# Kernel optimization log

Hardware: AMD Instinct MI355X
Metric: run time of the kernel (lower is better)

Reference implementation:

```python
import jax, jax.numpy as jnp
import numpy as np

EMBED = 1024

def setup_inputs() -> dict:
    key = jax.random.key(0)
    ks = jax.random.split(key, 10)
    s = 1.0 / np.sqrt(EMBED)
    inp = {
        "target": jax.random.normal(ks[0], (8, 2048, EMBED), dtype=jnp.float32),
        "source": jax.random.normal(ks[1], (8, 2048, EMBED), dtype=jnp.float32),
        "Wq": jax.random.uniform(ks[2], (EMBED, EMBED), jnp.float32, -s, s),
        "bq": jax.random.uniform(ks[3], (EMBED,), jnp.float32, -s, s),
        "Wk": jax.random.uniform(ks[4], (EMBED, EMBED), jnp.float32, -s, s),
        "bk": jax.random.uniform(ks[5], (EMBED,), jnp.float32, -s, s),
        "Wv": jax.random.uniform(ks[6], (EMBED, EMBED), jnp.float32, -s, s),
        "bv": jax.random.uniform(ks[7], (EMBED,), jnp.float32, -s, s),
        "Wo": jax.random.uniform(ks[8], (EMBED, EMBED), jnp.float32, -s, s),
        "bo": jax.random.uniform(ks[9], (EMBED,), jnp.float32, -s, s),
    }
    return inp

def reference(target, source, Wq, bq, Wk, bk, Wv, bv, Wo, bo):
    # Linear layers (torch Linear: x @ W.T + b)
    Q = jnp.einsum('btd,ed->bte', target, Wq) + bq   # [B, Tq, D]
    K = jnp.einsum('bsd,ed->bse', source, Wk) + bk   # [B, Tk, D]
    V = jnp.einsum('bsd,ed->bse', source, Wv) + bv   # [B, Tk, D]
    d_k = Q.shape[-1]
    scores = jnp.einsum('bte,bse->bts', Q, K) / jnp.sqrt(jnp.float32(d_k))  # [B, Tq, Tk]
    attn = jax.nn.softmax(scores, axis=-1)
    out = jnp.einsum('bts,bse->bte', attn, V)        # [B, Tq, D]
    return jnp.einsum('bte,oe->bto', out, Wo) + bo
```

## Files before the change

### kernel.cpp

```cpp
#include <hip/hip_runtime.h>
#include <stdint.h>

typedef unsigned short bf16_t;
typedef __attribute__((ext_vector_type(8))) short   short8;
typedef __attribute__((ext_vector_type(4))) float   floatx4;
typedef __attribute__((ext_vector_type(4))) unsigned int   uint4v;
typedef __attribute__((ext_vector_type(4))) unsigned short ushort4v;

#define GAS __attribute__((address_space(1)))
#define LAS __attribute__((address_space(3)))

__device__ __forceinline__ unsigned short f2bf(float f) {
  unsigned u = __float_as_uint(f);
  u += 0x7FFFu + ((u >> 16) & 1u);
  return (unsigned short)(u >> 16);
}

__device__ __forceinline__ void g2l16(const bf16_t* g, bf16_t* l) {
  __builtin_amdgcn_global_load_lds((const GAS uint32_t*)g, (LAS uint32_t*)l, 16, 0, 0);
}

__global__ __launch_bounds__(256) void conv_f32_bf16(const float* __restrict__ s,
                                                     bf16_t* __restrict__ d) {
  size_t i = ((size_t)blockIdx.x * 256 + threadIdx.x) * 4;
  float4 v = *(const float4*)(s + i);
  ushort4v o = { f2bf(v.x), f2bf(v.y), f2bf(v.z), f2bf(v.w) };
  *(ushort4v*)(d + i) = o;
}

__global__ __launch_bounds__(256) void conv_w(const float* __restrict__ w0, const float* __restrict__ w1,
                                              const float* __restrict__ w2, const float* __restrict__ w3,
                                              bf16_t* __restrict__ d) {
  const float* s = blockIdx.y == 0 ? w0 : blockIdx.y == 1 ? w1 : blockIdx.y == 2 ? w2 : w3;
  size_t i = ((size_t)blockIdx.x * 256 + threadIdx.x) * 4;
  float4 v = *(const float4*)(s + i);
  ushort4v o = { f2bf(v.x), f2bf(v.y), f2bf(v.z), f2bf(v.w) };
  *(ushort4v*)(d + (size_t)blockIdx.y * 1048576 + i) = o;
}

template <typename OutT>
__global__ __launch_bounds__(512, 2) void gemm256(
    const bf16_t* __restrict__ A, const bf16_t* __restrict__ B,
    const float* __restrict__ bias, OutT* __restrict__ C,
    int M, int N, int K, long aBat, long bBat, long cBat, float scale)
{
  const int tid  = threadIdx.x;
  const int lane = tid & 63;
  const int wv   = tid >> 6;

  int bx, by, bz;
  {
    const int gx = gridDim.x, gy = gridDim.y, gz = gridDim.z;
    const int nwg = gx * gy * gz;
    int flat = (blockIdx.z * gy + blockIdx.y) * gx + blockIdx.x;
    if ((nwg & 7) == 0) {
      const int q = nwg >> 3;
      flat = (flat & 7) * q + (flat >> 3);
    }
    bx = flat % gx;
    const int rem = flat / gx;
    by = rem % gy;
    bz = rem / gy;
  }
  const int bm = by * 256;
  const int bn = bx * 256;
  A += (size_t)bz * aBat;
  B += (size_t)bz * bBat;
  C += (size_t)bz * cBat;

  __shared__ bf16_t sm[65536];

  const int nt = K >> 6;

  const int wm = (wv >> 2) * 128;
  const int wn = (wv & 3) * 64;

  const int fr = lane & 15;
  const int kq = lane >> 4;
  const int chE = kq ^ ((fr >> 1) & 3);
  const unsigned fA = (unsigned)((wm + fr) * 32 + chE * 8);
  const unsigned fB = (unsigned)((wn + fr) * 32 + chE * 8);

  const unsigned c0    = (unsigned)((tid & 3) ^ ((tid >> 3) & 3));
  const unsigned soff  = (unsigned)((tid >> 2) * K + c0 * 8);
  const unsigned kx128 = (unsigned)(K << 7);
  const unsigned lOff  = (unsigned)(wv * 512 + lane * 8);

  const bf16_t* gA = A + (size_t)bm * K;
  const bf16_t* gB = B + (size_t)bn * K;

#define SMA(b, kh) (sm + (((b) << 1) | (kh)) * 8192)
#define SMB(b, kh) (sm + 32768 + (((b) << 1) | (kh)) * 8192)
#define STG(gbase, lbase)                                   \
  do {                                                      \
    g2l16((gbase) + soff,         (lbase) + lOff);          \
    g2l16((gbase) + soff + kx128, (lbase) + lOff + 4096);   \
  } while (0)

  floatx4 acc[8][4];
  floatx4 zero = {0.0f, 0.0f, 0.0f, 0.0f};
#pragma unroll
  for (int i = 0; i < 8; i++)
#pragma unroll
    for (int j = 0; j < 4; j++) acc[i][j] = zero;

  STG(gA,      SMA(0, 0));
  STG(gB,      SMB(0, 0));
  STG(gA + 32, SMA(0, 1));
  STG(gB + 32, SMB(0, 1));
  __syncthreads();

  int cur = 0;
  for (int t = 0; t < nt; ++t) {
    const int kc = t << 6;
    if (t + 1 < nt) {
      STG(gA + kc + 64, SMA(cur ^ 1, 0));
      STG(gB + kc + 64, SMB(cur ^ 1, 0));
      STG(gA + kc + 96, SMA(cur ^ 1, 1));
      STG(gB + kc + 96, SMB(cur ^ 1, 1));
    }
    const bf16_t* Ac0 = SMA(cur, 0);
    const bf16_t* Ac1 = SMA(cur, 1);
    const bf16_t* Bc0 = SMB(cur, 0);
    const bf16_t* Bc1 = SMB(cur, 1);
    short8 a_[4], b_[4];

#pragma unroll
    for (int i = 0; i < 4; i++) a_[i] = *(const short8*)(Ac0 + fA + i * 512);
#pragma unroll
    for (int i = 0; i < 4; i++) b_[i] = *(const short8*)(Bc0 + fB + i * 512);
#pragma unroll
    for (int mi = 0; mi < 4; mi++)
#pragma unroll
      for (int ni = 0; ni < 4; ni++)
        acc[mi][ni] = __builtin_amdgcn_mfma_f32_16x16x32_bf16(a_[mi], b_[ni], acc[mi][ni], 0, 0, 0);
    __builtin_amdgcn_sched_barrier(0);

#pragma unroll
    for (int i = 0; i < 4; i++) a_[i] = *(const short8*)(Ac0 + fA + (4 + i) * 512);
#pragma unroll
    for (int mi = 0; mi < 4; mi++)
#pragma unroll
      for (int ni = 0; ni < 4; ni++)
        acc[4 + mi][ni] = __builtin_amdgcn_mfma_f32_16x16x32_bf16(a_[mi], b_[ni], acc[4 + mi][ni], 0, 0, 0);
    __builtin_amdgcn_sched_barrier(0);

#pragma unroll
    for (int i = 0; i < 4; i++) a_[i] = *(const short8*)(Ac1 + fA + i * 512);
#pragma unroll
    for (int i = 0; i < 4; i++) b_[i] = *(const short8*)(Bc1 + fB + i * 512);
#pragma unroll
    for (int mi = 0; mi < 4; mi++)
#pragma unroll
      for (int ni = 0; ni < 4; ni++)
        acc[mi][ni] = __builtin_amdgcn_mfma_f32_16x16x32_bf16(a_[mi], b_[ni], acc[mi][ni], 0, 0, 0);
    __builtin_amdgcn_sched_barrier(0);

#pragma unroll
    for (int i = 0; i < 4; i++) a_[i] = *(const short8*)(Ac1 + fA + (4 + i) * 512);
#pragma unroll
    for (int mi = 0; mi < 4; mi++)
#pragma unroll
      for (int ni = 0; ni < 4; ni++)
        acc[4 + mi][ni] = __builtin_amdgcn_mfma_f32_16x16x32_bf16(a_[mi], b_[ni], acc[4 + mi][ni], 0, 0, 0);

    __syncthreads();
    cur ^= 1;
  }
#undef STG
#undef SMB
#undef SMA

  {
    const int er = (lane >> 4) * 4;
    const int ec = lane & 15;
    char* wreg = (char*)sm + wv * 16384;
#pragma unroll
    for (int pass = 0; pass < 2; ++pass) {
#pragma unroll
      for (int nf = 0; nf < 4; nf++) {
        const int lcol = nf * 16 + ec;
        const float bval = bias ? bias[bn + wn + lcol] : 0.0f;
#pragma unroll
        for (int mh = 0; mh < 4; mh++) {
#pragma unroll
          for (int r = 0; r < 4; r++) {
            float v = (acc[pass * 4 + mh][nf][r] + bval) * scale;
            const int row = mh * 16 + er + r;
            if constexpr (sizeof(OutT) == 4) {
              ((float*)wreg)[row * 64 + lcol] = v;
            } else {
              ((bf16_t*)wreg)[row * 64 + lcol] = f2bf(v);
            }
          }
        }
      }
      const size_t rbase = (size_t)(bm + wm + pass * 64);
      if constexpr (sizeof(OutT) == 4) {
        const float* tf = (const float*)wreg;
        float* Cf = (float*)C;
#pragma unroll
        for (int i = 0; i < 16; i++) {
          const int rr = i * 4 + (lane >> 4);
          floatx4 v = *(const floatx4*)(tf + rr * 64 + (lane & 15) * 4);
          *(floatx4*)(Cf + (rbase + rr) * N + bn + wn + (lane & 15) * 4) = v;
        }
      } else {
        const bf16_t* tb = (const bf16_t*)wreg;
        bf16_t* Cb = (bf16_t*)C;
#pragma unroll
        for (int i = 0; i < 8; i++) {
          const int rr = i * 8 + (lane >> 3);
          short8 v = *(const short8*)(tb + rr * 64 + (lane & 7) * 8);
          *(short8*)(Cb + (rbase + rr) * N + bn + wn + (lane & 7) * 8) = v;
        }
      }
    }
  }
}

__global__ __launch_bounds__(256) void softmax_rows(bf16_t* __restrict__ S) {
  const int tid = threadIdx.x;
  bf16_t* row = S + (size_t)blockIdx.x * 2048;
  uint4v raw = *(const uint4v*)(row + tid * 8);
  float x[8];
#pragma unroll
  for (int j = 0; j < 4; j++) {
    unsigned w = raw[j];
    x[2 * j]     = __uint_as_float(w << 16);
    x[2 * j + 1] = __uint_as_float(w & 0xFFFF0000u);
  }
  float m = -1e30f;
#pragma unroll
  for (int j = 0; j < 8; j++) m = fmaxf(m, x[j]);
  for (int o = 32; o > 0; o >>= 1) m = fmaxf(m, __shfl_xor(m, o, 64));
  __shared__ float red[4];
  if ((tid & 63) == 0) red[tid >> 6] = m;
  __syncthreads();
  m = fmaxf(fmaxf(red[0], red[1]), fmaxf(red[2], red[3]));

  float e[8];
  float s = 0.0f;
#pragma unroll
  for (int j = 0; j < 8; j++) { e[j] = __expf(x[j] - m); s += e[j]; }
  for (int o = 32; o > 0; o >>= 1) s += __shfl_xor(s, o, 64);
  __syncthreads();
  if ((tid & 63) == 0) red[tid >> 6] = s;
  __syncthreads();
  s = red[0] + red[1] + red[2] + red[3];
  float inv = 1.0f / s;

  uint4v o4;
#pragma unroll
  for (int j = 0; j < 4; j++) {
    unsigned lo = f2bf(e[2 * j] * inv);
    unsigned hi = f2bf(e[2 * j + 1] * inv);
    o4[j] = lo | (hi << 16);
  }
  *(uint4v*)(row + tid * 8) = o4;
}

__global__ __launch_bounds__(256) void transpose64(const bf16_t* __restrict__ V,
                                                   bf16_t* __restrict__ Vt) {
  __shared__ bf16_t t[64][72];
  const int tid = threadIdx.x;
  const int e0 = blockIdx.x * 64;
  const int s0 = blockIdx.y * 64;
  const size_t bb = (size_t)blockIdx.z * (2048 * 1024);
  const int r = tid >> 2;
  const int c = (tid & 3) * 16;
  const bf16_t* src = V + bb + (size_t)(s0 + r) * 1024 + e0 + c;
  uint4v v0 = *(const uint4v*)src;
  uint4v v1 = *(const uint4v*)(src + 8);
  *(uint4v*)&t[r][c]     = v0;
  *(uint4v*)&t[r][c + 8] = v1;
  __syncthreads();
  __attribute__((aligned(16))) bf16_t vals[16];
#pragma unroll
  for (int j = 0; j < 16; j++) vals[j] = t[c + j][r];
  bf16_t* dst = Vt + bb + (size_t)(e0 + r) * 2048 + s0 + c;
  *(uint4v*)dst       = *(const uint4v*)vals;
  *(uint4v*)(dst + 8) = *(const uint4v*)(vals + 8);
}

extern "C" void kernel_launch(void* const* d_in, const int* in_sizes, int n_in,
                              void* d_out, int out_size, void* d_ws, size_t ws_size,
                              hipStream_t stream) {
  const float* target = (const float*)d_in[0];
  const float* source = (const float*)d_in[1];
  const float* Wq = (const float*)d_in[2];
  const float* bq = (const float*)d_in[3];
  const float* Wk = (const float*)d_in[4];
  const float* bk = (const float*)d_in[5];
  const float* Wv = (const float*)d_in[6];
  const float* bv = (const float*)d_in[7];
  const float* Wo = (const float*)d_in[8];
  const float* bo = (const float*)d_in[9];
  float* out = (float*)d_out;

  char* ws = (char*)d_ws;
  bf16_t* Qb  = (bf16_t*)(ws + 0);
  bf16_t* Kb  = (bf16_t*)(ws + 33554432);
  bf16_t* Vt  = (bf16_t*)(ws + 67108864);
  bf16_t* Wb  = (bf16_t*)(ws + 100663296);
  bf16_t* Tb  = (bf16_t*)(ws + 109051904);
  bf16_t* Sb  = Tb;
  bf16_t* Srb = (bf16_t*)(ws + 142606336);
  bf16_t* Vb  = (bf16_t*)(ws + 176160768);
  bf16_t* AO  = Vb;

  conv_f32_bf16<<<16384, 256, 0, stream>>>(target, Tb);
  conv_f32_bf16<<<16384, 256, 0, stream>>>(source, Srb);
  conv_w<<<dim3(1024, 4), 256, 0, stream>>>(Wq, Wk, Wv, Wo, Wb);

  gemm256<<<dim3(4, 64, 1), 512, 0, stream>>>(Tb,  Wb,           bq, Qb, 16384, 1024, 1024, 0L, 0L, 0L, 0.03125f);
  gemm256<<<dim3(4, 64, 1), 512, 0, stream>>>(Srb, Wb + 1048576, bk, Kb, 16384, 1024, 1024, 0L, 0L, 0L, 1.0f);
  gemm256<<<dim3(4, 64, 1), 512, 0, stream>>>(Srb, Wb + 2097152, bv, Vb, 16384, 1024, 1024, 0L, 0L, 0L, 1.0f);

  transpose64<<<dim3(16, 32, 8), 256, 0, stream>>>(Vb, Vt);

  gemm256<<<dim3(8, 8, 8), 512, 0, stream>>>(Qb, Kb, (const float*)nullptr, Sb,
      2048, 2048, 1024, (long)2048 * 1024, (long)2048 * 1024, (long)2048 * 2048, 1.0f);

  softmax_rows<<<16384, 256, 0, stream>>>(Sb);

  gemm256<<<dim3(4, 8, 8), 512, 0, stream>>>(Sb, Vt, (const float*)nullptr, AO,
      2048, 1024, 2048, (long)2048 * 2048, (long)1024 * 2048, (long)2048 * 1024, 1.0f);

  gemm256<<<dim3(4, 64, 1), 512, 0, stream>>>(AO, Wb + 3145728, bo, out,
      16384, 1024, 1024, 0L, 0L, 0L, 1.0f);
}
```

Before: 509.3 us.

## Interleave prefetch loads with MFMA phases using fine-grained barriers and priority

Splits the next-tile global-to-LDS prefetch into four pieces issued between the four MFMA sub-phases instead of all at the top of the loop. Replaces the per-iteration __syncthreads with explicit s_barrier plus partial vmcnt/lgkmcnt waits, and raises wave priority around MFMA clusters so waves stay aligned in a ping-pong schedule. The aim is to hide global load latency and spread LDS/VMEM traffic across compute. It adds many barriers per iteration, and the hand-written waitcnt counts must match the number of outstanding loads or correctness breaks.

Result: no change. 516.9 us (+1.5%).

```diff
diff --git a/kernel.cpp b/kernel.cpp
--- a/kernel.cpp
+++ b/kernel.cpp
@@ -19,6 +19,9 @@
 __device__ __forceinline__ void g2l16(const bf16_t* g, bf16_t* l) {
   __builtin_amdgcn_global_load_lds((const GAS uint32_t*)g, (LAS uint32_t*)l, 16, 0, 0);
 }
+
+#define SB0() __builtin_amdgcn_sched_barrier(0)
+#define BARX() do { SB0(); __builtin_amdgcn_s_barrier(); SB0(); } while (0)
 
 __global__ __launch_bounds__(256) void conv_f32_bf16(const float* __restrict__ s,
                                                      bf16_t* __restrict__ d) {
@@ -108,17 +111,14 @@
   STG(gB,      SMB(0, 0));
   STG(gA + 32, SMA(0, 1));
   STG(gB + 32, SMB(0, 1));
-  __syncthreads();
+  SB0();
+  asm volatile("s_waitcnt vmcnt(4)");
+  BARX();
 
   int cur = 0;
   for (int t = 0; t < nt; ++t) {
     const int kc = t << 6;
-    if (t + 1 < nt) {
-      STG(gA + kc + 64, SMA(cur ^ 1, 0));
-      STG(gB + kc + 64, SMB(cur ^ 1, 0));
-      STG(gA + kc + 96, SMA(cur ^ 1, 1));
-      STG(gB + kc + 96, SMB(cur ^ 1, 1));
-    }
+    const bool pf = (t + 1 < nt);
     const bf16_t* Ac0 = SMA(cur, 0);
     const bf16_t* Ac1 = SMA(cur, 1);
     const bf16_t* Bc0 = SMB(cur, 0);
@@ -129,47 +129,78 @@
     for (int i = 0; i < 4; i++) a_[i] = *(const short8*)(Ac0 + fA + i * 512);
 #pragma unroll
     for (int i = 0; i < 4; i++) b_[i] = *(const short8*)(Bc0 + fB + i * 512);
+    if (pf) STG(gA + kc + 64, SMA(cur ^ 1, 0));
+    BARX();
+    asm volatile("s_waitcnt lgkmcnt(0)");
+    SB0();
+    __builtin_amdgcn_s_setprio(1);
 #pragma unroll
     for (int mi = 0; mi < 4; mi++)
 #pragma unroll
       for (int ni = 0; ni < 4; ni++)
         acc[mi][ni] = __builtin_amdgcn_mfma_f32_16x16x32_bf16(a_[mi], b_[ni], acc[mi][ni], 0, 0, 0);
-    __builtin_amdgcn_sched_barrier(0);
+    __builtin_amdgcn_s_setprio(0);
+    BARX();
 
 #pragma unroll
     for (int i = 0; i < 4; i++) a_[i] = *(const short8*)(Ac0 + fA + (4 + i) * 512);
+    if (pf) STG(gB + kc + 64, SMB(cur ^ 1, 0));
+    SB0();
+    if (pf) asm volatile("s_waitcnt vmcnt(4)");
+    else    asm volatile("s_waitcnt vmcnt(0)");
+    BARX();
+    asm volatile("s_waitcnt lgkmcnt(0)");
+    SB0();
+    __builtin_amdgcn_s_setprio(1);
 #pragma unroll
     for (int mi = 0; mi < 4; mi++)
 #pragma unroll
       for (int ni = 0; ni < 4; ni++)
         acc[4 + mi][ni] = __builtin_amdgcn_mfma_f32_16x16x32_bf16(a_[mi], b_[ni], acc[4 + mi][ni], 0, 0, 0);
-    __builtin_amdgcn_sched_barrier(0);
+    __builtin_amdgcn_s_setprio(0);
+    BARX();
 
 #pragma unroll
     for (int i = 0; i < 4; i++) a_[i] = *(const short8*)(Ac1 + fA + i * 512);
 #pragma unroll
     for (int i = 0; i < 4; i++) b_[i] = *(const short8*)(Bc1 + fB + i * 512);
+    if (pf) STG(gA + kc + 96, SMA(cur ^ 1, 1));
+    BARX();
+    asm volatile("s_waitcnt lgkmcnt(0)");
+    SB0();
+    __builtin_amdgcn_s_setprio(1);
 #pragma unroll
     for (int mi = 0; mi < 4; mi++)
 #pragma unroll
       for (int ni = 0; ni < 4; ni++)
         acc[mi][ni] = __builtin_amdgcn_mfma_f32_16x16x32_bf16(a_[mi], b_[ni], acc[mi][ni], 0, 0, 0);
-    __builtin_amdgcn_sched_barrier(0);
+    __builtin_amdgcn_s_setprio(0);
+    BARX();
 
 #pragma unroll
     for (int i = 0; i < 4; i++) a_[i] = *(const short8*)(Ac1 + fA + (4 + i) * 512);
+    if (pf) STG(gB + kc + 96, SMB(cur ^ 1, 1));
+    BARX();
+    asm volatile("s_waitcnt lgkmcnt(0)");
+    SB0();
+    __builtin_amdgcn_s_setprio(1);
 #pragma unroll
     for (int mi = 0; mi < 4; mi++)
 #pragma unroll
       for (int ni = 0; ni < 4; ni++)
         acc[4 + mi][ni] = __builtin_amdgcn_mfma_f32_16x16x32_bf16(a_[mi], b_[ni], acc[4 + mi][ni], 0, 0, 0);
-
-    __syncthreads();
+    __builtin_amdgcn_s_setprio(0);
+    SB0();
+    if (pf) asm volatile("s_waitcnt vmcnt(4)");
+    BARX();
+
     cur ^= 1;
   }
 #undef STG
 #undef SMB
 #undef SMA
+
+  __syncthreads();
 
   {
     const int er = (lane >> 4) * 4;
```
